# Kernel optimization log

Hardware: AMD Instinct MI355X
Metric: run time of the kernel (lower is better)

The kernel has to match this reference:

```python
import jax, jax.numpy as jnp
import numpy as np

N = 50000
E = 800000
K = 3


def _cheb_edge_weights(edge_index, n):
    # PyG ChebConv __norm__ with normalization='sym', lambda_max=2.0:
    # L_hat = 2/lambda_max * (I - D^-1/2 A D^-1/2) - I = -D^-1/2 A D^-1/2 (zero diag)
    row, col = edge_index[0], edge_index[1]
    deg = jax.ops.segment_sum(jnp.ones((edge_index.shape[1],), jnp.float32), row, num_segments=n)
    dis = jnp.where(deg > 0, jax.lax.rsqrt(jnp.maximum(deg, 1.0)), 0.0)
    return -dis[row] * dis[col]


def _cheb_conv(x, edge_index, w_edge, W, b, n):
    # W: [K, in, out]; Chebyshev recurrence T0=x, T1=L_hat x, Tk=2 L_hat T_{k-1} - T_{k-2}
    src, dst = edge_index[0], edge_index[1]

    def prop(h):
        return jax.ops.segment_sum(h[src] * w_edge[:, None], dst, num_segments=n)

    Tx0 = x
    out = Tx0 @ W[0]
    Tx1 = prop(Tx0)
    out = out + Tx1 @ W[1]
    for k in range(2, W.shape[0]):
        Tx2 = 2.0 * prop(Tx1) - Tx0
        out = out + Tx2 @ W[k]
        Tx0, Tx1 = Tx1, Tx2
    return out + b


def setup_inputs() -> dict:
    key = jax.random.key(0)
    ks = jax.random.split(key, 8)
    x = jax.random.normal(ks[0], (N, 64), dtype=jnp.float32)
    edge_index = jax.random.randint(ks[1], (2, E), 0, N, dtype=jnp.int64)
    s = 0.1
    W1 = jax.random.normal(ks[2], (K, 64, 64), dtype=jnp.float32) * s
    b1 = jnp.zeros((64,), jnp.float32)
    W2 = jax.random.normal(ks[3], (K, 64, 64), dtype=jnp.float32) * s
    b2 = jnp.zeros((64,), jnp.float32)
    W3 = jax.random.normal(ks[4], (K, 64, 32), dtype=jnp.float32) * s
    b3 = jnp.zeros((32,), jnp.float32)
    return {"x": x, "edge_index": edge_index, "W1": W1, "b1": b1,
            "W2": W2, "b2": b2, "W3": W3, "b3": b3}


def reference(x, edge_index, W1, b1, W2, b2, W3, b3):
    n = x.shape[0]
    w_edge = _cheb_edge_weights(edge_index, n)
    h = jax.nn.relu(_cheb_conv(x, edge_index, w_edge, W1, b1, n))  # dropout p=0 -> identity
    h = jax.nn.relu(_cheb_conv(h, edge_index, w_edge, W2, b2, n))
    return _cheb_conv(h, edge_index, w_edge, W3, b3, n)
```

## Files before the change

### kernel.cpp

```cpp
#include <hip/hip_runtime.h>

#define NB 128
#define NWMAX 16384
#define LSTR 72

typedef __attribute__((ext_vector_type(8))) short bf16x8;
typedef __attribute__((ext_vector_type(4))) float f32x4;

__device__ __forceinline__ unsigned bfr(float x) {
    unsigned u = __float_as_uint(x);
    return (u + 0x7FFFu + ((u >> 16) & 1u)) >> 16;
}
__device__ __forceinline__ unsigned pack2(float lo, float hi) {
    return bfr(lo) | (bfr(hi) << 16);
}
__device__ __forceinline__ float ubf_lo(unsigned q) { return __uint_as_float(q << 16); }
__device__ __forceinline__ float ubf_hi(unsigned q) { return __uint_as_float(q & 0xFFFF0000u); }


__global__ void __launch_bounds__(256) k_hist(const int* __restrict__ ei, int E, int chunk,
                                              int NW, unsigned* __restrict__ partialS,
                                              unsigned* __restrict__ partialD) {
    __shared__ unsigned lS[NWMAX];
    __shared__ unsigned lD[NWMAX];
    for (int w = threadIdx.x; w < NW; w += 256) { lS[w] = 0u; lD[w] = 0u; }
    __syncthreads();
    int e0 = blockIdx.x * chunk;
    int e1 = e0 + chunk; if (e1 > E) e1 = E;
    for (int e = e0 + threadIdx.x; e < e1; e += 256) {
        int s = ei[e], d = ei[E + e];
        atomicAdd(&lS[s >> 2], 1u << ((s & 3) * 8));
        atomicAdd(&lD[d >> 2], 1u << ((d & 3) * 8));
    }
    __syncthreads();
    unsigned* pS = partialS + (size_t)blockIdx.x * NW;
    unsigned* pD = partialD + (size_t)blockIdx.x * NW;
    for (int w = threadIdx.x; w < NW; w += 256) { pS[w] = lS[w]; pD[w] = lD[w]; }
}

__global__ void __launch_bounds__(256) k_red(const unsigned* __restrict__ partialS,
                                             const unsigned* __restrict__ partialD,
                                             unsigned* __restrict__ baseM, int NW, int n,
                                             float* __restrict__ dis,
                                             unsigned* __restrict__ cnt,
                                             ushort* __restrict__ slot, int CAP) {
    int w = blockIdx.x * 256 + threadIdx.x;
    if (w >= NW) return;
    unsigned s0 = 0, s1 = 0, s2 = 0, s3 = 0;
    unsigned c0 = 0, c1 = 0, c2 = 0, c3 = 0;
#pragma unroll 8
    for (int b = 0; b < NB; b++) {
        unsigned vs = partialS[(size_t)b * NW + w];
        unsigned vd = partialD[(size_t)b * NW + w];
        baseM[(size_t)b * NW + w] = c0 | (c1 << 8) | (c2 << 16) | (c3 << 24);
        s0 += vs & 0xFF; s1 += (vs >> 8) & 0xFF; s2 += (vs >> 16) & 0xFF; s3 += vs >> 24;
        c0 += vd & 0xFF; c1 += (vd >> 8) & 0xFF; c2 += (vd >> 16) & 0xFF; c3 += vd >> 24;
    }
    unsigned ss[4] = {s0, s1, s2, s3}, cc[4] = {c0, c1, c2, c3};
    int node0 = w * 4;
    if (node0 + 3 < n) {
        ((float4*)dis)[w] = make_float4(s0 ? 1.0f / sqrtf((float)s0) : 0.0f,
                                        s1 ? 1.0f / sqrtf((float)s1) : 0.0f,
                                        s2 ? 1.0f / sqrtf((float)s2) : 0.0f,
                                        s3 ? 1.0f / sqrtf((float)s3) : 0.0f);
        ((uint4*)cnt)[w] = make_uint4(c0, c1, c2, c3);
    } else {
        for (int j = 0; j < 4 && node0 + j < n; j++) {
            dis[node0 + j] = ss[j] ? 1.0f / sqrtf((float)ss[j]) : 0.0f;
            cnt[node0 + j] = cc[j];
        }
    }
#pragma unroll
    for (int j = 0; j < 4; j++) {
        int node = node0 + j;
        if (node >= n) break;
        int c = (int)cc[j]; if (c > CAP) c = CAP;
        int c4 = (c + 3) & ~3; if (c4 > CAP) c4 = CAP;
        for (int e = c; e < c4; e++) slot[(size_t)node * CAP + e] = (ushort)n;
    }
}

__global__ void __launch_bounds__(256) k_build3(const int* __restrict__ ei, int E, int chunk,
                                                int NW, const unsigned* __restrict__ baseM,
                                                ushort* __restrict__ slot, int CAP,
                                                const float* __restrict__ x,
                                                const float* __restrict__ dis,
                                                uint2* __restrict__ g0,
                                                uint2* __restrict__ g1,
                                                uint2* __restrict__ xb0,
                                                const float* __restrict__ W1,
                                                const float* __restrict__ W2,
                                                const float* __restrict__ W3,
                                                ushort* __restrict__ Wb, int n) {
    __shared__ unsigned cur[NWMAX];
    __shared__ unsigned bs[NWMAX];
    if ((int)blockIdx.x < NB) {
        const unsigned* bRow = baseM + (size_t)blockIdx.x * NW;
        for (int w = threadIdx.x; w < NW; w += 256) { cur[w] = 0u; bs[w] = bRow[w]; }
        __syncthreads();
        int e0 = blockIdx.x * chunk;
        int e1 = e0 + chunk; if (e1 > E) e1 = E;
        for (int e = e0 + threadIdx.x; e < e1; e += 256) {
            int s = ei[e], d = ei[E + e];
            int w = d >> 2, sh = (d & 3) * 8;
            unsigned rank = (atomicAdd(&cur[w], 1u << sh) >> sh) & 0xFF;
            unsigned pos = ((bs[w] >> sh) & 0xFF) + rank;
            if (pos < (unsigned)CAP) slot[(size_t)d * CAP + pos] = (ushort)s;
        }
        return;
    }
    int nblk = gridDim.x - NB;
    int bid = (int)blockIdx.x - NB;
    int tot = (n + 1) * 16;
    for (int i = bid * 256 + threadIdx.x; i < tot; i += nblk * 256) {
        if (i >= n * 16) {
            g0[i] = make_uint2(0u, 0u);
            g1[i] = make_uint2(0u, 0u);
            continue;
        }
        int node = i >> 4;
        float s = dis[node];
        float4 v = ((const float4*)x)[i];
        xb0[i] = make_uint2(pack2(v.x, v.y), pack2(v.z, v.w));
        g0[i]  = make_uint2(pack2(s * v.x, s * v.y), pack2(s * v.z, s * v.w));
    }
    for (int idx = bid * 256 + threadIdx.x; idx < (24 + 24 + 12) * 64; idx += nblk * 256) {
        const float* W; int OUTC, NCT, f; ushort* dst; int id = idx;
        if (id < 24 * 64)      { W = W1; OUTC = 64; NCT = 4; dst = Wb;            f = id >> 6; }
        else if (id < 48 * 64) { W = W2; OUTC = 64; NCT = 4; dst = Wb + 24 * 512; f = (id >> 6) - 24; }
        else                   { W = W3; OUTC = 32; NCT = 2; dst = Wb + 48 * 512; f = (id >> 6) - 48; }
        int l = id & 63;
        int ks = f / NCT, ct = f - ks * NCT;
        int col = ct * 16 + (l & 15);
        int k0 = ks * 32 + (l >> 4) * 8;
        unsigned pk[4];
        for (int jj = 0; jj < 4; jj++) {
            unsigned lohi[2];
            for (int h = 0; h < 2; h++) {
                int k = k0 + jj * 2 + h;
                int seg = k >> 6, r = k & 63;
                float v;
                if (seg == 0)      v = W[r * OUTC + col] - W[(128 + r) * OUTC + col];
                else if (seg == 1) v = W[(64 + r) * OUTC + col];
                else               v = 2.0f * W[(128 + r) * OUTC + col];
                lohi[h] = bfr(v);
            }
            pk[jj] = lohi[0] | (lohi[1] << 16);
        }
        *(uint4*)(dst + ((size_t)f * 64 + l) * 8) = make_uint4(pk[0], pk[1], pk[2], pk[3]);
    }
}


struct Acc8 { float a0, a1, a2, a3, a4, a5, a6, a7; };

__device__ __forceinline__ void acc8(Acc8& A, uint4 v) {
    A.a0 += ubf_lo(v.x); A.a1 += ubf_hi(v.x);
    A.a2 += ubf_lo(v.y); A.a3 += ubf_hi(v.y);
    A.a4 += ubf_lo(v.z); A.a5 += ubf_hi(v.z);
    A.a6 += ubf_lo(v.w); A.a7 += ubf_hi(v.w);
}

__device__ __forceinline__ Acc8 gather_sum(const uint4* __restrict__ gsrc,
                                           const ushort* __restrict__ base, int m4, int j) {
    Acc8 A = {0.f, 0.f, 0.f, 0.f, 0.f, 0.f, 0.f, 0.f};
    int e = 0;
    for (; e + 8 <= m4; e += 8) {
        uint2 qa = *(const uint2*)(base + e);
        uint2 qb = *(const uint2*)(base + e + 4);
        uint4 v0 = gsrc[(size_t)(qa.x & 0xFFFFu) * 8 + j];
        uint4 v1 = gsrc[(size_t)(qa.x >> 16) * 8 + j];
        uint4 v2 = gsrc[(size_t)(qa.y & 0xFFFFu) * 8 + j];
        uint4 v3 = gsrc[(size_t)(qa.y >> 16) * 8 + j];
        uint4 v4 = gsrc[(size_t)(qb.x & 0xFFFFu) * 8 + j];
        uint4 v5 = gsrc[(size_t)(qb.x >> 16) * 8 + j];
        uint4 v6 = gsrc[(size_t)(qb.y & 0xFFFFu) * 8 + j];
        uint4 v7 = gsrc[(size_t)(qb.y >> 16) * 8 + j];
        acc8(A, v0); acc8(A, v1); acc8(A, v2); acc8(A, v3);
        acc8(A, v4); acc8(A, v5); acc8(A, v6); acc8(A, v7);
    }
    if (e < m4) {
        uint2 qa = *(const uint2*)(base + e);
        uint4 v0 = gsrc[(size_t)(qa.x & 0xFFFFu) * 8 + j];
        uint4 v1 = gsrc[(size_t)(qa.x >> 16) * 8 + j];
        uint4 v2 = gsrc[(size_t)(qa.y & 0xFFFFu) * 8 + j];
        uint4 v3 = gsrc[(size_t)(qa.y >> 16) * 8 + j];
        acc8(A, v0); acc8(A, v1); acc8(A, v2); acc8(A, v3);
    }
    return A;
}


__global__ void __launch_bounds__(256) k_prop(const uint4* __restrict__ gsrc,
                                              const unsigned* __restrict__ cnt,
                                              const ushort* __restrict__ slot,
                                              const float* __restrict__ dis,
                                              uint4* __restrict__ xbout,
                                              uint4* __restrict__ gout, int n, int CAP) {
    const int j = threadIdx.x & 7;
    const int node = blockIdx.x * 32 + (threadIdx.x >> 3);
    if (node >= n) return;
    int m = (int)cnt[node]; if (m > CAP) m = CAP;
    int m4 = (m + 3) & ~3;  if (m4 > CAP) m4 = CAP;
    Acc8 A = gather_sum(gsrc, slot + (size_t)node * CAP, m4, j);
    float s = dis[node];
    float f0 = -s * A.a0, f1 = -s * A.a1, f2 = -s * A.a2, f3 = -s * A.a3;
    float f4 = -s * A.a4, f5 = -s * A.a5, f6 = -s * A.a6, f7 = -s * A.a7;
    xbout[(size_t)node * 8 + j] =
        make_uint4(pack2(f0, f1), pack2(f2, f3), pack2(f4, f5), pack2(f6, f7));
    gout[(size_t)node * 8 + j] =
        make_uint4(pack2(s * f0, s * f1), pack2(s * f2, s * f3),
                   pack2(s * f4, s * f5), pack2(s * f6, s * f7));
}

template <int NCT, bool RELU, bool WG>
__global__ void __launch_bounds__(256) k_pm(const uint4* __restrict__ gsrc,
                                            const unsigned* __restrict__ cnt,
                                            const ushort* __restrict__ slot,
                                            const float* __restrict__ dis,
                                            const ushort* __restrict__ X0,
                                            const ushort* __restrict__ X1,
                                            const ushort* __restrict__ Wb,
                                            const float* __restrict__ bias,
                                            float* __restrict__ outf,
                                            ushort* __restrict__ xbout,
                                            ushort* __restrict__ gout, int n, int CAP) {
    constexpr int OUTC = NCT * 16;
    __shared__ ushort P2[32 * LSTR];
    const int r0 = blockIdx.x * 32;

    {
        const int j = threadIdx.x & 7;
        const int ni = threadIdx.x >> 3;
        const int node = r0 + ni;
        uint4 pk = make_uint4(0u, 0u, 0u, 0u);
        if (node < n) {
            int m = (int)cnt[node]; if (m > CAP) m = CAP;
            int m4 = (m + 3) & ~3;  if (m4 > CAP) m4 = CAP;
            Acc8 A = gather_sum(gsrc, slot + (size_t)node * CAP, m4, j);
            float s = dis[node];
            pk = make_uint4(pack2(-s * A.a0, -s * A.a1), pack2(-s * A.a2, -s * A.a3),
                            pack2(-s * A.a4, -s * A.a5), pack2(-s * A.a6, -s * A.a7));
        }
        *(uint4*)&P2[ni * LSTR + j * 8] = pk;
    }
    __syncthreads();

    const int wv = threadIdx.x >> 6;
    if (wv >= NCT) return;
    const int ct = wv;
    const int l = threadIdx.x & 63;
    const int lm = l & 15, lh = l >> 4, koff = lh * 8;
    const int rA0 = (r0 + lm < n) ? r0 + lm : n - 1;
    const int rA1 = (r0 + 16 + lm < n) ? r0 + 16 + lm : n - 1;

    float bv = bias[ct * 16 + lm];
    f32x4 c0 = {bv, bv, bv, bv}, c1 = c0;

#pragma unroll
    for (int kt = 0; kt < 2; kt++) {
        bf16x8 a0 = *(const bf16x8*)(X0 + (size_t)rA0 * 64 + kt * 32 + koff);
        bf16x8 a1 = *(const bf16x8*)(X0 + (size_t)rA1 * 64 + kt * 32 + koff);
        bf16x8 b = *(const bf16x8*)(Wb + ((size_t)(kt * NCT + ct) * 64 + l) * 8);
        c0 = __builtin_amdgcn_mfma_f32_16x16x32_bf16(a0, b, c0, 0, 0, 0);
        c1 = __builtin_amdgcn_mfma_f32_16x16x32_bf16(a1, b, c1, 0, 0, 0);
    }
#pragma unroll
    for (int kt = 0; kt < 2; kt++) {
        bf16x8 a0 = *(const bf16x8*)(X1 + (size_t)rA0 * 64 + kt * 32 + koff);
        bf16x8 a1 = *(const bf16x8*)(X1 + (size_t)rA1 * 64 + kt * 32 + koff);
        bf16x8 b = *(const bf16x8*)(Wb + ((size_t)((2 + kt) * NCT + ct) * 64 + l) * 8);
        c0 = __builtin_amdgcn_mfma_f32_16x16x32_bf16(a0, b, c0, 0, 0, 0);
        c1 = __builtin_amdgcn_mfma_f32_16x16x32_bf16(a1, b, c1, 0, 0, 0);
    }
#pragma unroll
    for (int kt = 0; kt < 2; kt++) {
        bf16x8 a0 = *(const bf16x8*)&P2[lm * LSTR + kt * 32 + koff];
        bf16x8 a1 = *(const bf16x8*)&P2[(16 + lm) * LSTR + kt * 32 + koff];
        bf16x8 b = *(const bf16x8*)(Wb + ((size_t)((4 + kt) * NCT + ct) * 64 + l) * 8);
        c0 = __builtin_amdgcn_mfma_f32_16x16x32_bf16(a0, b, c0, 0, 0, 0);
        c1 = __builtin_amdgcn_mfma_f32_16x16x32_bf16(a1, b, c1, 0, 0, 0);
    }

#pragma unroll
    for (int half = 0; half < 2; half++) {
        int rbase = r0 + half * 16 + lh * 4;
        int col = ct * 16 + lm;
#pragma unroll
        for (int r = 0; r < 4; r++) {
            int row = rbase + r;
            if (row < n) {
                float v = half ? c1[r] : c0[r];
                if (RELU) v = fmaxf(v, 0.0f);
                if (WG) {
                    float s = dis[row];
                    xbout[(size_t)row * OUTC + col] = (ushort)bfr(v);
                    gout[(size_t)row * OUTC + col] = (ushort)bfr(s * v);
                } else {
                    outf[(size_t)row * OUTC + col] = v;
                }
            }
        }
    }
}


extern "C" void kernel_launch(void* const* d_in, const int* in_sizes, int n_in,
                              void* d_out, int out_size, void* d_ws, size_t ws_size,
                              hipStream_t stream) {
    const float* x  = (const float*)d_in[0];
    const int*   ei = (const int*)d_in[1];
    const float* W1 = (const float*)d_in[2];
    const float* b1 = (const float*)d_in[3];
    const float* W2 = (const float*)d_in[4];
    const float* b2 = (const float*)d_in[5];
    const float* W3 = (const float*)d_in[6];
    const float* b3 = (const float*)d_in[7];
    float* out = (float*)d_out;

    const int n = in_sizes[0] / 64;
    const int E = in_sizes[1] / 2;
    const int NW = (n + 3) >> 2;
    const int chunk = (E + NB - 1) / NB;

    char* wsp = (char*)d_ws;
    size_t off = 0;
    auto alloc = [&](size_t bytes) -> char* {
        char* p = wsp + off;
        off += (bytes + 255) & ~(size_t)255;
        return p;
    };
    float* dis     = (float*)alloc((size_t)n * 4);
    unsigned* cnt  = (unsigned*)alloc((size_t)n * 4);
    const size_t XB  = (size_t)n * 64 * 2;
    const size_t XBP = (size_t)(n + 1) * 64 * 2;
    ushort* xb0 = (ushort*)alloc(XB);
    ushort* xbA = (ushort*)alloc(XB);
    ushort* xbC = (ushort*)alloc(XB);
    ushort* xbD = (ushort*)alloc(XB);
    ushort* g0  = (ushort*)alloc(XBP);
    ushort* g1  = (ushort*)alloc(XBP);
    ushort* Wb  = (ushort*)alloc((size_t)60 * 512 * 2);

    unsigned* baseM    = (unsigned*)xbA;
    unsigned* partialS = (unsigned*)xbC;
    unsigned* partialD = (unsigned*)xbD;

    size_t leftover = (ws_size > off) ? (ws_size - off) : 0;
    int CAP = (int)(leftover / ((size_t)n * 2));
    if (CAP > 64) CAP = 64;
    if (CAP < 16) CAP = 16;
    CAP &= ~3;
    ushort* slot = (ushort*)alloc((size_t)n * CAP * 2);

    const int nb_red  = (NW + 255) / 256;
    const int nb_prop = (n + 31) / 32;

    k_hist<<<NB, 256, 0, stream>>>(ei, E, chunk, NW, partialS, partialD);
    k_red<<<nb_red, 256, 0, stream>>>(partialS, partialD, baseM, NW, n, dis, cnt, slot, CAP);
    k_build3<<<NB + 128, 256, 0, stream>>>(ei, E, chunk, NW, baseM, slot, CAP,
                                           x, dis, (uint2*)g0, (uint2*)g1, (uint2*)xb0,
                                           W1, W2, W3, Wb, n);

    k_prop<<<nb_prop, 256, 0, stream>>>((uint4*)g0, cnt, slot, dis, (uint4*)xbA,
                                        (uint4*)g1, n, CAP);
    k_pm<4, true, true><<<nb_prop, 256, 0, stream>>>((uint4*)g1, cnt, slot, dis, xb0, xbA,
                                                     Wb, b1, nullptr, xbC, g0, n, CAP);

    k_prop<<<nb_prop, 256, 0, stream>>>((uint4*)g0, cnt, slot, dis, (uint4*)xbA,
                                        (uint4*)g1, n, CAP);
    k_pm<4, true, true><<<nb_prop, 256, 0, stream>>>((uint4*)g1, cnt, slot, dis, xbC, xbA,
                                                     Wb + 24 * 512, b2, nullptr, xbD, g0,
                                                     n, CAP);

    k_prop<<<nb_prop, 256, 0, stream>>>((uint4*)g0, cnt, slot, dis, (uint4*)xbA,
                                        (uint4*)g1, n, CAP);
    k_pm<2, false, false><<<nb_prop, 256, 0, stream>>>((uint4*)g1, cnt, slot, dis, xbD, xbA,
                                                       Wb + 48 * 512, b3, out, nullptr,
                                                       nullptr, n, CAP);
}
```

Baseline: 174.0 us.

## Split gather source into two feature-half planes and process two halves per thread

The scaled bf16 feature buffers g0/g1 move from node-major 64-wide rows to two separate planes, each holding 32 features per node. Propagation threads now handle 64 nodes per block with 4 lanes per node, looping over the two planes. Each plane is half the size, so random gathers should hit a smaller working set in cache. The MFMA stage is reorganised to cover 64 rows per block across all four waves, and CAP is rounded to a multiple of 8 so neighbor slots can be read as uint4. In exchange, each thread reads the neighbor index list twice, once per plane, and issues twice as many dependent gather loops.

```diff
diff --git a/kernel.cpp b/kernel.cpp
--- a/kernel.cpp
+++ b/kernel.cpp
@@ -94,6 +94,7 @@
                                                 ushort* __restrict__ Wb, int n) {
     __shared__ unsigned cur[NWMAX];
     __shared__ unsigned bs[NWMAX];
+    const int np1 = n + 1;
     if ((int)blockIdx.x < NB) {
         const unsigned* bRow = baseM + (size_t)blockIdx.x * NW;
         for (int w = threadIdx.x; w < NW; w += 256) { cur[w] = 0u; bs[w] = bRow[w]; }
@@ -111,18 +112,20 @@
     }
     int nblk = gridDim.x - NB;
     int bid = (int)blockIdx.x - NB;
-    int tot = (n + 1) * 16;
+    int tot = np1 * 16;
     for (int i = bid * 256 + threadIdx.x; i < tot; i += nblk * 256) {
+        int node = i >> 4, fp = i & 15;
+        int h = fp >> 3, f4 = fp & 7;
+        size_t gidx = ((size_t)h * np1 + node) * 8 + f4;
         if (i >= n * 16) {
-            g0[i] = make_uint2(0u, 0u);
-            g1[i] = make_uint2(0u, 0u);
+            g0[gidx] = make_uint2(0u, 0u);
+            g1[gidx] = make_uint2(0u, 0u);
             continue;
         }
-        int node = i >> 4;
         float s = dis[node];
         float4 v = ((const float4*)x)[i];
         xb0[i] = make_uint2(pack2(v.x, v.y), pack2(v.z, v.w));
-        g0[i]  = make_uint2(pack2(s * v.x, s * v.y), pack2(s * v.z, s * v.w));
+        g0[gidx] = make_uint2(pack2(s * v.x, s * v.y), pack2(s * v.z, s * v.w));
     }
     for (int idx = bid * 256 + threadIdx.x; idx < (24 + 24 + 12) * 64; idx += nblk * 256) {
         const float* W; int OUTC, NCT, f; ushort* dst; int id = idx;
@@ -161,30 +164,29 @@
     A.a6 += ubf_lo(v.w); A.a7 += ubf_hi(v.w);
 }
 
-__device__ __forceinline__ Acc8 gather_sum(const uint4* __restrict__ gsrc,
-                                           const ushort* __restrict__ base, int m4, int j) {
+__device__ __forceinline__ Acc8 gather4(const uint4* __restrict__ gH,
+                                        const ushort* __restrict__ base, int m4) {
     Acc8 A = {0.f, 0.f, 0.f, 0.f, 0.f, 0.f, 0.f, 0.f};
     int e = 0;
     for (; e + 8 <= m4; e += 8) {
-        uint2 qa = *(const uint2*)(base + e);
-        uint2 qb = *(const uint2*)(base + e + 4);
-        uint4 v0 = gsrc[(size_t)(qa.x & 0xFFFFu) * 8 + j];
-        uint4 v1 = gsrc[(size_t)(qa.x >> 16) * 8 + j];
-        uint4 v2 = gsrc[(size_t)(qa.y & 0xFFFFu) * 8 + j];
-        uint4 v3 = gsrc[(size_t)(qa.y >> 16) * 8 + j];
-        uint4 v4 = gsrc[(size_t)(qb.x & 0xFFFFu) * 8 + j];
-        uint4 v5 = gsrc[(size_t)(qb.x >> 16) * 8 + j];
-        uint4 v6 = gsrc[(size_t)(qb.y & 0xFFFFu) * 8 + j];
-        uint4 v7 = gsrc[(size_t)(qb.y >> 16) * 8 + j];
+        uint4 q = *(const uint4*)(base + e);
+        uint4 v0 = gH[(size_t)(q.x & 0xFFFFu) * 4];
+        uint4 v1 = gH[(size_t)(q.x >> 16) * 4];
+        uint4 v2 = gH[(size_t)(q.y & 0xFFFFu) * 4];
+        uint4 v3 = gH[(size_t)(q.y >> 16) * 4];
+        uint4 v4 = gH[(size_t)(q.z & 0xFFFFu) * 4];
+        uint4 v5 = gH[(size_t)(q.z >> 16) * 4];
+        uint4 v6 = gH[(size_t)(q.w & 0xFFFFu) * 4];
+        uint4 v7 = gH[(size_t)(q.w >> 16) * 4];
         acc8(A, v0); acc8(A, v1); acc8(A, v2); acc8(A, v3);
         acc8(A, v4); acc8(A, v5); acc8(A, v6); acc8(A, v7);
     }
     if (e < m4) {
-        uint2 qa = *(const uint2*)(base + e);
-        uint4 v0 = gsrc[(size_t)(qa.x & 0xFFFFu) * 8 + j];
-        uint4 v1 = gsrc[(size_t)(qa.x >> 16) * 8 + j];
-        uint4 v2 = gsrc[(size_t)(qa.y & 0xFFFFu) * 8 + j];
-        uint4 v3 = gsrc[(size_t)(qa.y >> 16) * 8 + j];
+        uint2 q = *(const uint2*)(base + e);
+        uint4 v0 = gH[(size_t)(q.x & 0xFFFFu) * 4];
+        uint4 v1 = gH[(size_t)(q.x >> 16) * 4];
+        uint4 v2 = gH[(size_t)(q.y & 0xFFFFu) * 4];
+        uint4 v3 = gH[(size_t)(q.y >> 16) * 4];
         acc8(A, v0); acc8(A, v1); acc8(A, v2); acc8(A, v3);
     }
     return A;
@@ -197,20 +199,24 @@
                                               const float* __restrict__ dis,
                                               uint4* __restrict__ xbout,
                                               uint4* __restrict__ gout, int n, int CAP) {
-    const int j = threadIdx.x & 7;
-    const int node = blockIdx.x * 32 + (threadIdx.x >> 3);
+    const int j = threadIdx.x & 3;
+    const int node = blockIdx.x * 64 + (threadIdx.x >> 2);
     if (node >= n) return;
+    const int np1 = n + 1;
     int m = (int)cnt[node]; if (m > CAP) m = CAP;
     int m4 = (m + 3) & ~3;  if (m4 > CAP) m4 = CAP;
-    Acc8 A = gather_sum(gsrc, slot + (size_t)node * CAP, m4, j);
+    const ushort* base = slot + (size_t)node * CAP;
     float s = dis[node];
-    float f0 = -s * A.a0, f1 = -s * A.a1, f2 = -s * A.a2, f3 = -s * A.a3;
-    float f4 = -s * A.a4, f5 = -s * A.a5, f6 = -s * A.a6, f7 = -s * A.a7;
-    xbout[(size_t)node * 8 + j] =
-        make_uint4(pack2(f0, f1), pack2(f2, f3), pack2(f4, f5), pack2(f6, f7));
-    gout[(size_t)node * 8 + j] =
-        make_uint4(pack2(s * f0, s * f1), pack2(s * f2, s * f3),
-                   pack2(s * f4, s * f5), pack2(s * f6, s * f7));
+    for (int h = 0; h < 2; h++) {
+        Acc8 A = gather4(gsrc + ((size_t)h * np1) * 4 + j, base, m4);
+        float f0 = -s * A.a0, f1 = -s * A.a1, f2 = -s * A.a2, f3 = -s * A.a3;
+        float f4 = -s * A.a4, f5 = -s * A.a5, f6 = -s * A.a6, f7 = -s * A.a7;
+        xbout[(size_t)node * 8 + h * 4 + j] =
+            make_uint4(pack2(f0, f1), pack2(f2, f3), pack2(f4, f5), pack2(f6, f7));
+        gout[((size_t)h * np1 + node) * 4 + j] =
+            make_uint4(pack2(s * f0, s * f1), pack2(s * f2, s * f3),
+                       pack2(s * f4, s * f5), pack2(s * f6, s * f7));
+    }
 }
 
 template <int NCT, bool RELU, bool WG>
@@ -226,78 +232,93 @@
                                             ushort* __restrict__ xbout,
                                             ushort* __restrict__ gout, int n, int CAP) {
     constexpr int OUTC = NCT * 16;
-    __shared__ ushort P2[32 * LSTR];
-    const int r0 = blockIdx.x * 32;
+    __shared__ ushort P2[64 * LSTR];
+    const int r0 = blockIdx.x * 64;
+    const int np1 = n + 1;
 
     {
-        const int j = threadIdx.x & 7;
-        const int ni = threadIdx.x >> 3;
+        const int j = threadIdx.x & 3;
+        const int ni = threadIdx.x >> 2;
         const int node = r0 + ni;
-        uint4 pk = make_uint4(0u, 0u, 0u, 0u);
+        int m4 = 0;
+        const ushort* base = slot;
+        float s = 0.0f;
         if (node < n) {
             int m = (int)cnt[node]; if (m > CAP) m = CAP;
-            int m4 = (m + 3) & ~3;  if (m4 > CAP) m4 = CAP;
-            Acc8 A = gather_sum(gsrc, slot + (size_t)node * CAP, m4, j);
-            float s = dis[node];
-            pk = make_uint4(pack2(-s * A.a0, -s * A.a1), pack2(-s * A.a2, -s * A.a3),
-                            pack2(-s * A.a4, -s * A.a5), pack2(-s * A.a6, -s * A.a7));
-        }
-        *(uint4*)&P2[ni * LSTR + j * 8] = pk;
+            m4 = (m + 3) & ~3; if (m4 > CAP) m4 = CAP;
+            base = slot + (size_t)node * CAP;
+            s = dis[node];
+        }
+        for (int h = 0; h < 2; h++) {
+            uint4 pk = make_uint4(0u, 0u, 0u, 0u);
+            if (node < n) {
+                Acc8 A = gather4(gsrc + ((size_t)h * np1) * 4 + j, base, m4);
+                pk = make_uint4(pack2(-s * A.a0, -s * A.a1), pack2(-s * A.a2, -s * A.a3),
+                                pack2(-s * A.a4, -s * A.a5), pack2(-s * A.a6, -s * A.a7));
+            }
+            *(uint4*)&P2[ni * LSTR + h * 32 + j * 8] = pk;
+        }
     }
     __syncthreads();
 
-    const int wv = threadIdx.x >> 6;
-    if (wv >= NCT) return;
-    const int ct = wv;
+    const int w = threadIdx.x >> 6;
     const int l = threadIdx.x & 63;
     const int lm = l & 15, lh = l >> 4, koff = lh * 8;
-    const int rA0 = (r0 + lm < n) ? r0 + lm : n - 1;
-    const int rA1 = (r0 + 16 + lm < n) ? r0 + 16 + lm : n - 1;
-
-    float bv = bias[ct * 16 + lm];
-    f32x4 c0 = {bv, bv, bv, bv}, c1 = c0;
-
-#pragma unroll
-    for (int kt = 0; kt < 2; kt++) {
-        bf16x8 a0 = *(const bf16x8*)(X0 + (size_t)rA0 * 64 + kt * 32 + koff);
-        bf16x8 a1 = *(const bf16x8*)(X0 + (size_t)rA1 * 64 + kt * 32 + koff);
-        bf16x8 b = *(const bf16x8*)(Wb + ((size_t)(kt * NCT + ct) * 64 + l) * 8);
-        c0 = __builtin_amdgcn_mfma_f32_16x16x32_bf16(a0, b, c0, 0, 0, 0);
-        c1 = __builtin_amdgcn_mfma_f32_16x16x32_bf16(a1, b, c1, 0, 0, 0);
-    }
-#pragma unroll
-    for (int kt = 0; kt < 2; kt++) {
-        bf16x8 a0 = *(const bf16x8*)(X1 + (size_t)rA0 * 64 + kt * 32 + koff);
-        bf16x8 a1 = *(const bf16x8*)(X1 + (size_t)rA1 * 64 + kt * 32 + koff);
-        bf16x8 b = *(const bf16x8*)(Wb + ((size_t)((2 + kt) * NCT + ct) * 64 + l) * 8);
-        c0 = __builtin_amdgcn_mfma_f32_16x16x32_bf16(a0, b, c0, 0, 0, 0);
-        c1 = __builtin_amdgcn_mfma_f32_16x16x32_bf16(a1, b, c1, 0, 0, 0);
-    }
-#pragma unroll
-    for (int kt = 0; kt < 2; kt++) {
-        bf16x8 a0 = *(const bf16x8*)&P2[lm * LSTR + kt * 32 + koff];
-        bf16x8 a1 = *(const bf16x8*)&P2[(16 + lm) * LSTR + kt * 32 + koff];
-        bf16x8 b = *(const bf16x8*)(Wb + ((size_t)((4 + kt) * NCT + ct) * 64 + l) * 8);
-        c0 = __builtin_amdgcn_mfma_f32_16x16x32_bf16(a0, b, c0, 0, 0, 0);
-        c1 = __builtin_amdgcn_mfma_f32_16x16x32_bf16(a1, b, c1, 0, 0, 0);
-    }
-
-#pragma unroll
-    for (int half = 0; half < 2; half++) {
-        int rbase = r0 + half * 16 + lh * 4;
-        int col = ct * 16 + lm;
-#pragma unroll
-        for (int r = 0; r < 4; r++) {
-            int row = rbase + r;
-            if (row < n) {
-                float v = half ? c1[r] : c0[r];
-                if (RELU) v = fmaxf(v, 0.0f);
-                if (WG) {
-                    float s = dis[row];
-                    xbout[(size_t)row * OUTC + col] = (ushort)bfr(v);
-                    gout[(size_t)row * OUTC + col] = (ushort)bfr(s * v);
-                } else {
-                    outf[(size_t)row * OUTC + col] = v;
+
+    for (int t = w; t < 2 * NCT; t += 4) {
+        const int rg = t / NCT, ct = t % NCT;
+        const int rb = r0 + rg * 32;
+        if (rb >= n) continue;
+        const int rA0 = (rb + lm < n) ? rb + lm : n - 1;
+        const int rA1 = (rb + 16 + lm < n) ? rb + 16 + lm : n - 1;
+        const int lr0 = rg * 32 + lm, lr1 = rg * 32 + 16 + lm;
+
+        float bv = bias[ct * 16 + lm];
+        f32x4 c0 = {bv, bv, bv, bv}, c1 = c0;
+
+#pragma unroll
+        for (int kt = 0; kt < 2; kt++) {
+            bf16x8 a0 = *(const bf16x8*)(X0 + (size_t)rA0 * 64 + kt * 32 + koff);
+            bf16x8 a1 = *(const bf16x8*)(X0 + (size_t)rA1 * 64 + kt * 32 + koff);
+            bf16x8 b = *(const bf16x8*)(Wb + ((size_t)(kt * NCT + ct) * 64 + l) * 8);
+            c0 = __builtin_amdgcn_mfma_f32_16x16x32_bf16(a0, b, c0, 0, 0, 0);
+            c1 = __builtin_amdgcn_mfma_f32_16x16x32_bf16(a1, b, c1, 0, 0, 0);
+        }
+#pragma unroll
+        for (int kt = 0; kt < 2; kt++) {
+            bf16x8 a0 = *(const bf16x8*)(X1 + (size_t)rA0 * 64 + kt * 32 + koff);
+            bf16x8 a1 = *(const bf16x8*)(X1 + (size_t)rA1 * 64 + kt * 32 + koff);
+            bf16x8 b = *(const bf16x8*)(Wb + ((size_t)((2 + kt) * NCT + ct) * 64 + l) * 8);
+            c0 = __builtin_amdgcn_mfma_f32_16x16x32_bf16(a0, b, c0, 0, 0, 0);
+            c1 = __builtin_amdgcn_mfma_f32_16x16x32_bf16(a1, b, c1, 0, 0, 0);
+        }
+#pragma unroll
+        for (int kt = 0; kt < 2; kt++) {
+            bf16x8 a0 = *(const bf16x8*)&P2[lr0 * LSTR + kt * 32 + koff];
+            bf16x8 a1 = *(const bf16x8*)&P2[lr1 * LSTR + kt * 32 + koff];
+            bf16x8 b = *(const bf16x8*)(Wb + ((size_t)((4 + kt) * NCT + ct) * 64 + l) * 8);
+            c0 = __builtin_amdgcn_mfma_f32_16x16x32_bf16(a0, b, c0, 0, 0, 0);
+            c1 = __builtin_amdgcn_mfma_f32_16x16x32_bf16(a1, b, c1, 0, 0, 0);
+        }
+
+#pragma unroll
+        for (int half = 0; half < 2; half++) {
+            int rbase = rb + half * 16 + lh * 4;
+            int col = ct * 16 + lm;
+#pragma unroll
+            for (int r = 0; r < 4; r++) {
+                int row = rbase + r;
+                if (row < n) {
+                    float v = half ? c1[r] : c0[r];
+                    if (RELU) v = fmaxf(v, 0.0f);
+                    if (WG) {
+                        float s = dis[row];
+                        xbout[(size_t)row * OUTC + col] = (ushort)bfr(v);
+                        int hh = col >> 5, cw = col & 31;
+                        gout[((size_t)hh * np1 + row) * 32 + cw] = (ushort)bfr(s * v);
+                    } else {
+                        outf[(size_t)row * OUTC + col] = v;
+                    }
                 }
             }
         }
@@ -350,11 +371,11 @@
     int CAP = (int)(leftover / ((size_t)n * 2));
     if (CAP > 64) CAP = 64;
     if (CAP < 16) CAP = 16;
-    CAP &= ~3;
+    CAP &= ~7;
     ushort* slot = (ushort*)alloc((size_t)n * CAP * 2);
 
     const int nb_red  = (NW + 255) / 256;
-    const int nb_prop = (n + 31) / 32;
+    const int nb_np   = (n + 63) / 64;
 
     k_hist<<<NB, 256, 0, stream>>>(ei, E, chunk, NW, partialS, partialD);
     k_red<<<nb_red, 256, 0, stream>>>(partialS, partialD, baseM, NW, n, dis, cnt, slot, CAP);
@@ -362,20 +383,20 @@
                                            x, dis, (uint2*)g0, (uint2*)g1, (uint2*)xb0,
                                            W1, W2, W3, Wb, n);
 
-    k_prop<<<nb_prop, 256, 0, stream>>>((uint4*)g0, cnt, slot, dis, (uint4*)xbA,
-                                        (uint4*)g1, n, CAP);
-    k_pm<4, true, true><<<nb_prop, 256, 0, stream>>>((uint4*)g1, cnt, slot, dis, xb0, xbA,
-                                                     Wb, b1, nullptr, xbC, g0, n, CAP);
-
-    k_prop<<<nb_prop, 256, 0, stream>>>((uint4*)g0, cnt, slot, dis, (uint4*)xbA,
-                                        (uint4*)g1, n, CAP);
-    k_pm<4, true, true><<<nb_prop, 256, 0, stream>>>((uint4*)g1, cnt, slot, dis, xbC, xbA,
-                                                     Wb + 24 * 512, b2, nullptr, xbD, g0,
-                                                     n, CAP);
-
-    k_prop<<<nb_prop, 256, 0, stream>>>((uint4*)g0, cnt, slot, dis, (uint4*)xbA,
-                                        (uint4*)g1, n, CAP);
-    k_pm<2, false, false><<<nb_prop, 256, 0, stream>>>((uint4*)g1, cnt, slot, dis, xbD, xbA,
-                                                       Wb + 48 * 512, b3, out, nullptr,
-                                                       nullptr, n, CAP);
-}
+    k_prop<<<nb_np, 256, 0, stream>>>((uint4*)g0, cnt, slot, dis, (uint4*)xbA,
+                                      (uint4*)g1, n, CAP);
+    k_pm<4, true, true><<<nb_np, 256, 0, stream>>>((uint4*)g1, cnt, slot, dis, xb0, xbA,
+                                                   Wb, b1, nullptr, xbC, g0, n, CAP);
+
+    k_prop<<<nb_np, 256, 0, stream>>>((uint4*)g0, cnt, slot, dis, (uint4*)xbA,
+                                      (uint4*)g1, n, CAP);
+    k_pm<4, true, true><<<nb_np, 256, 0, stream>>>((uint4*)g1, cnt, slot, dis, xbC, xbA,
+                                                   Wb + 24 * 512, b2, nullptr, xbD, g0,
+                                                   n, CAP);
+
+    k_prop<<<nb_np, 256, 0, stream>>>((uint4*)g0, cnt, slot, dis, (uint4*)xbA,
+                                      (uint4*)g1, n, CAP);
+    k_pm<2, false, false><<<nb_np, 256, 0, stream>>>((uint4*)g1, cnt, slot, dis, xbD, xbA,
+                                                     Wb + 48 * 512, b3, out, nullptr,
+                                                     nullptr, n, CAP);
+}
```

Result: slower. 196.2 us (+12.8%).
